# Performance work log

Hardware: AMD Instinct MI355X
Metric: run time of the kernel (lower is better)

Reference implementation:

```python
import jax, jax.numpy as jnp
import numpy as np

N_NOTES = 4096
SIZE = 64
N_EDGE_TYPE = 14  # len(GRAPH_KEYS) * 2
N_ITER = 5


def setup_inputs() -> dict:
    key = jax.random.key(0)
    ks = jax.random.split(key, 12)
    xav = np.sqrt(2.0 / (SIZE + SIZE))  # xavier_normal_ std for square [SIZE,SIZE]
    x = jax.random.normal(ks[0], (N_NOTES, SIZE), dtype=jnp.float32)
    # sparse binary adjacency per edge type (avg degree ~8) to keep gate
    # pre-activations in a sane range, as a real score graph would be
    edge_matrix = (jax.random.uniform(ks[1], (N_EDGE_TYPE, N_NOTES, N_NOTES)) < 0.002).astype(jnp.float32)
    wz = jax.random.normal(ks[2], (N_EDGE_TYPE, SIZE, SIZE), dtype=jnp.float32) * xav
    wr = jax.random.normal(ks[3], (N_EDGE_TYPE, SIZE, SIZE), dtype=jnp.float32) * xav
    wh = jax.random.normal(ks[4], (N_EDGE_TYPE, SIZE, SIZE), dtype=jnp.float32) * xav
    uz = jax.random.normal(ks[5], (SIZE, SIZE), dtype=jnp.float32) * xav
    ur = jax.random.normal(ks[6], (SIZE, SIZE), dtype=jnp.float32) * xav
    uh = jax.random.normal(ks[7], (SIZE, SIZE), dtype=jnp.float32) * xav
    bz = jnp.zeros((SIZE,), dtype=jnp.float32)
    br = jnp.zeros((SIZE,), dtype=jnp.float32)
    bh = jnp.zeros((SIZE,), dtype=jnp.float32)
    return {"x": x, "edge_matrix": edge_matrix, "wz": wz, "wr": wr, "wh": wh,
            "uz": uz, "ur": ur, "uh": uh, "bz": bz, "br": br, "bh": bh}


def reference(x, edge_matrix, wz, wr, wh, uz, ur, uh, bz, br, bh):
    # Faithful GatedGraph.forward: 5 iterations of edge-typed message passing
    # with GRU-style gates and the (unusual, but as-written) blend
    #   h <- (1 - z) * h + r * h_tilde
    h = x  # [N, D]
    for _ in range(N_ITER):
        # activation[e, n, d] = sum_m edge[e, m, n] * h[m, d]  (edge_matrix.transpose(1,2) @ h)
        act = jnp.einsum('emn,md->end', edge_matrix, h)  # [E, N, D]
        az = jnp.einsum('end,edf->nf', act, wz)  # bmm(act, wz).sum(0)
        ar = jnp.einsum('end,edf->nf', act, wr)
        ah = jnp.einsum('end,edf->nf', act, wh)
        z = jax.nn.sigmoid(az + h @ uz + bz)
        r = jax.nn.sigmoid(ar + h @ ur + br)
        h_tilde = jnp.tanh(ah + (r * h) @ uh + bh)
        h = (1.0 - z) * h + r * h_tilde
    return h
```

## Files before the change

### kernel.cpp

```cpp
#include <hip/hip_runtime.h>
#include <hip/hip_bf16.h>
#include <cstdint>

#define N_NOTES 4096
#define SIZE 64
#define NE 14
#define NITER 5
#define MAXDEG 64
#define KTOT 960
#define ASTR 968
#define HPAD 4113
#define PWN 184320
#define PUN 4096

typedef __attribute__((ext_vector_type(8))) short short8;
typedef __attribute__((ext_vector_type(4))) float float4v;

__device__ __forceinline__ ushort f2bf(float f){
  union{float f; uint32_t u;} x; x.f=f;
  uint32_t r = x.u + 0x7fffu + ((x.u>>16)&1u);
  return (ushort)(r>>16);
}
__device__ __forceinline__ float bf2f(ushort h){
  union{uint32_t u; float f;} x; x.u=((uint32_t)h)<<16; return x.f;
}
__device__ __forceinline__ void split_bf(float v, ushort& hi, ushort& lo){
  hi = f2bf(v);
  lo = f2bf(v - bf2f(hi));
}

__global__ __launch_bounds__(256) void k_zero(int* __restrict__ deg, uint32_t* __restrict__ adj32,
                                              float* __restrict__ h0pad, float* __restrict__ h1pad){
  int i = blockIdx.x*256 + threadIdx.x;
  if (i < NE*N_NOTES) deg[i] = 0;
  for (int j = i; j < NE*N_NOTES*MAXDEG/2; j += gridDim.x*256)
    adj32[j] = 0x10101010u;
  if (i < (HPAD-N_NOTES)*SIZE){ h0pad[i] = 0.f; h1pad[i] = 0.f; }
}

__global__ __launch_bounds__(256) void k_build(const float4v* __restrict__ edge4,
                                               int* __restrict__ deg,
                                               ushort* __restrict__ adj){
  int row = blockIdx.x;
  int e = row >> 12, m = row & 4095;
  const float4v* p = edge4 + (size_t)row * (N_NOTES/4);
  int t = threadIdx.x;
  #pragma unroll
  for (int i=0;i<4;i++){
    int idx4 = t + i*256;
    float4v v = p[idx4];
    int nbase = idx4*4;
    #pragma unroll
    for (int j=0;j<4;j++){
      if (v[j] != 0.0f){
        int n = nbase + j;
        int slot = atomicAdd(&deg[(e<<12)+n], 1);
        if (slot < MAXDEG) adj[(size_t)((e<<12)+n)*MAXDEG + slot] = (ushort)m;
      }
    }
  }
}

__global__ __launch_bounds__(256) void k_pack(const float* __restrict__ wz, const float* __restrict__ wr,
                                              const float* __restrict__ wh, const float* __restrict__ uz,
                                              const float* __restrict__ ur, const float* __restrict__ uh,
                                              ushort* __restrict__ PWH, ushort* __restrict__ PWL,
                                              ushort* __restrict__ PUH, ushort* __restrict__ PUL){
  int idx = blockIdx.x*256 + threadIdx.x;
  if (idx < PWN){
    int j = idx & 7, lane = (idx>>3)&63, t = idx>>9;
    int kk = t % 30, wg = t/30; int w = wg & 3, g = wg >> 2;
    int col = g*64 + w*16 + (lane&15);
    int k = kk*32 + ((lane>>4)<<3) + j;
    int e = k >> 6, d = k & 63, f = col & 63;
    float v;
    if (e < NE){
      const float* wp = (g==0)?wz:(g==1)?wr:wh;
      v = wp[(e*64 + d)*64 + f];
    } else {
      v = (g==0) ? uz[d*64+f] : (g==1) ? ur[d*64+f] : 0.0f;
    }
    ushort hi,lo; split_bf(v,hi,lo);
    PWH[idx]=hi; PWL[idx]=lo;
  } else if (idx < PWN + PUN){
    int i2 = idx - PWN;
    int j = i2 & 7, lane = (i2>>3)&63, t = i2>>9;
    int kk = t & 1, w = t >> 1;
    int col = w*16 + (lane&15);
    int k = kk*32 + ((lane>>4)<<3) + j;
    float v = uh[k*64 + col];
    ushort hi,lo; split_bf(v,hi,lo);
    PUH[i2]=hi; PUL[i2]=lo;
  }
}

__global__ __launch_bounds__(256) void k_fused(const int* __restrict__ deg, const ushort* __restrict__ adj,
                                               const ushort* __restrict__ PWH, const ushort* __restrict__ PWL,
                                               const ushort* __restrict__ PUH, const ushort* __restrict__ PUL,
                                               const float* __restrict__ bz, const float* __restrict__ br,
                                               const float* __restrict__ bh,
                                               const float* __restrict__ hin, float* __restrict__ hout,
                                               float* __restrict__ out, int last){
  __shared__ ushort aHs[16*ASTR];
  __shared__ ushort aLs[16*ASTR];

  const int tid  = threadIdx.x;
  const int w    = tid >> 6;
  const int lane = tid & 63;
  const int qi   = lane >> 4;
  const int ql   = lane & 15;
  const int r0   = blockIdx.x * 16;
  const float4v* hin4 = (const float4v*)hin;

  const int ri = w*4 + qi;
  const int n  = r0 + ri;

  int dgv[NE]; int mvv[NE];
  #pragma unroll
  for (int e=0;e<NE;e++){
    int base = (e<<12) + n;
    dgv[e] = deg[base];
    mvv[e] = adj[(size_t)base*MAXDEG + ql];
  }
  #pragma unroll
  for (int p=0; p<15; ++p){
    float4v a0={0.f,0.f,0.f,0.f}, a1={0.f,0.f,0.f,0.f};
    float4v a2={0.f,0.f,0.f,0.f}, a3={0.f,0.f,0.f,0.f};
    if (p < NE){
      #pragma unroll
      for (int k=0;k<16;k+=4){
        int m0 = __shfl(mvv[p], qi*16 + k);
        int m1 = __shfl(mvv[p], qi*16 + k+1);
        int m2 = __shfl(mvv[p], qi*16 + k+2);
        int m3 = __shfl(mvv[p], qi*16 + k+3);
        a0 += hin4[m0*16 + ql];
        a1 += hin4[m1*16 + ql];
        a2 += hin4[m2*16 + ql];
        a3 += hin4[m3*16 + ql];
      }
      int dg = dgv[p];
      if (dg > 16){
        size_t base = (size_t)((p<<12)+n)*MAXDEG;
        for (int k=16;k<dg;k++){
          int m = adj[base + k];
          a0 += hin4[m*16 + ql];
        }
      }
    } else {
      a0 = hin4[n*16 + ql];
    }
    float4v acc = (a0 + a1) + (a2 + a3);
    ushort h0,h1,h2,h3,l0,l1,l2,l3;
    split_bf(acc[0],h0,l0); split_bf(acc[1],h1,l1);
    split_bf(acc[2],h2,l2); split_bf(acc[3],h3,l3);
    int o = ri*ASTR + p*64 + ql*4;
    *(ushort4*)&aHs[o] = make_ushort4(h0,h1,h2,h3);
    *(ushort4*)&aLs[o] = make_ushort4(l0,l1,l2,l3);
  }
  __syncthreads();

  const int l15  = lane & 15;
  const int koff = (lane >> 4) * 8;
  const int colf = w*16 + l15;
  float4v acc[3];
  #pragma unroll
  for (int g=0;g<3;g++) acc[g] = (float4v){0.f,0.f,0.f,0.f};
  #pragma unroll 3
  for (int kk=0; kk<30; ++kk){
    short8 aH = *(const short8*)&aHs[l15*ASTR + kk*32 + koff];
    short8 aL = *(const short8*)&aLs[l15*ASTR + kk*32 + koff];
    #pragma unroll
    for (int g=0; g<3; ++g){
      int boff = (((g*4 + w)*30 + kk) << 9) + lane*8;
      short8 bH = *(const short8*)(PWH + boff);
      short8 bL = *(const short8*)(PWL + boff);
      acc[g] = __builtin_amdgcn_mfma_f32_16x16x32_bf16(aH,bH,acc[g],0,0,0);
      acc[g] = __builtin_amdgcn_mfma_f32_16x16x32_bf16(aH,bL,acc[g],0,0,0);
      acc[g] = __builtin_amdgcn_mfma_f32_16x16x32_bf16(aL,bH,acc[g],0,0,0);
    }
  }
  __syncthreads();

  ushort* rhH = aHs;
  ushort* rhL = aHs + 16*72;
  const int crow0 = (lane>>4)*4;
  const float brf = br[colf];
  float hrow[4], rreg[4];
  #pragma unroll
  for (int i=0;i<4;i++){
    float hv = hin[(size_t)(r0+crow0+i)*64 + colf];
    hrow[i] = hv;
    float r = 1.f/(1.f + expf(-(acc[1][i] + brf)));
    rreg[i] = r;
    ushort hi,lo; split_bf(r*hv,hi,lo);
    rhH[(crow0+i)*72 + colf] = hi;
    rhL[(crow0+i)*72 + colf] = lo;
  }
  __syncthreads();

  float4v acc2 = {0.f,0.f,0.f,0.f};
  #pragma unroll
  for (int kk=0; kk<2; ++kk){
    short8 aH = *(const short8*)&rhH[l15*72 + kk*32 + koff];
    short8 aL = *(const short8*)&rhL[l15*72 + kk*32 + koff];
    int boff = (((w<<1) + kk) << 9) + lane*8;
    short8 bH = *(const short8*)(PUH + boff);
    short8 bL = *(const short8*)(PUL + boff);
    acc2 = __builtin_amdgcn_mfma_f32_16x16x32_bf16(aH,bH,acc2,0,0,0);
    acc2 = __builtin_amdgcn_mfma_f32_16x16x32_bf16(aH,bL,acc2,0,0,0);
    acc2 = __builtin_amdgcn_mfma_f32_16x16x32_bf16(aL,bH,acc2,0,0,0);
  }

  const float bzf = bz[colf], bhf = bh[colf];
  #pragma unroll
  for (int i=0;i<4;i++){
    float z  = 1.f/(1.f + expf(-(acc[0][i] + bzf)));
    float ht = tanhf(acc[2][i] + acc2[i] + bhf);
    float hn = (1.f - z)*hrow[i] + rreg[i]*ht;
    size_t idx = (size_t)(r0+crow0+i)*64 + colf;
    hout[idx] = hn;
    if (last) out[idx] = hn;
  }
}

extern "C" void kernel_launch(void* const* d_in, const int* in_sizes, int n_in,
                              void* d_out, int out_size, void* d_ws, size_t ws_size,
                              hipStream_t stream) {
  const float* x    = (const float*)d_in[0];
  const float* edge = (const float*)d_in[1];
  const float* wz   = (const float*)d_in[2];
  const float* wr   = (const float*)d_in[3];
  const float* wh   = (const float*)d_in[4];
  const float* uz   = (const float*)d_in[5];
  const float* ur   = (const float*)d_in[6];
  const float* uh   = (const float*)d_in[7];
  const float* bz   = (const float*)d_in[8];
  const float* br   = (const float*)d_in[9];
  const float* bh   = (const float*)d_in[10];
  float* out = (float*)d_out;

  char* ws = (char*)d_ws;
  size_t off = 0;
  auto alloc = [&](size_t bytes)->void*{
    void* p = ws + off;
    off = (off + bytes + 255) & ~(size_t)255;
    return p;
  };
  const size_t EN = (size_t)NE * N_NOTES;
  const size_t ND = (size_t)N_NOTES * SIZE;
  int*    deg  = (int*)   alloc(EN * 4);
  ushort* adj  = (ushort*)alloc(EN * MAXDEG * 2);
  ushort* PWH  = (ushort*)alloc((size_t)PWN * 2);
  ushort* PWL  = (ushort*)alloc((size_t)PWN * 2);
  ushort* PUH  = (ushort*)alloc((size_t)PUN * 2);
  ushort* PUL  = (ushort*)alloc((size_t)PUN * 2);
  float*  h0   = (float*) alloc((size_t)HPAD * SIZE * 4);
  float*  h1   = (float*) alloc((size_t)HPAD * SIZE * 4);

  k_zero <<<2048, 256, 0, stream>>>(deg, (uint32_t*)adj,
                                    h0 + ND, h1 + ND);
  k_build<<<NE*N_NOTES, 256, 0, stream>>>((const float4v*)edge, deg, adj);
  k_pack <<<(PWN + PUN)/256, 256, 0, stream>>>(wz, wr, wh, uz, ur, uh, PWH, PWL, PUH, PUL);
  hipMemcpyAsync(h0, x, ND*4, hipMemcpyDeviceToDevice, stream);

  float* hcur = h0;
  float* hnxt = h1;
  for (int it = 0; it < NITER; ++it){
    k_fused<<<N_NOTES/16, 256, 0, stream>>>(deg, adj, PWH, PWL, PUH, PUL,
                                            bz, br, bh, hcur, hnxt,
                                            out, (it == NITER-1) ? 1 : 0);
    float* t = hcur; hcur = hnxt; hnxt = t;
  }
}
```

Measured before the change: 326.7 us.

## Split fused GRU step across 16 waves with K-split MFMA and LDS reduction

Grows the block from 4 to 16 waves per 16-row tile. The gather work of 240 (edge, row) pairs is spread across all waves, and the 30-step K loop of the gate GEMM is split four ways. Partial sums are then reduced through shared memory before the gate nonlinearities. This aims to raise parallelism and latency hiding per tile, at the cost of extra LDS traffic, two more barriers, and a tail where only 4 waves do the Uh MFMA and output.

After: 285.7 us. 12.6% less time.

```diff
diff --git a/kernel.cpp b/kernel.cpp
--- a/kernel.cpp
+++ b/kernel.cpp
@@ -12,6 +12,7 @@
 #define HPAD 4113
 #define PWN 184320
 #define PUN 4096
+#define PSTR 264
 
 typedef __attribute__((ext_vector_type(8))) short short8;
 typedef __attribute__((ext_vector_type(4))) float float4v;
@@ -69,8 +70,8 @@
   int idx = blockIdx.x*256 + threadIdx.x;
   if (idx < PWN){
     int j = idx & 7, lane = (idx>>3)&63, t = idx>>9;
-    int kk = t % 30, wg = t/30; int w = wg & 3, g = wg >> 2;
-    int col = g*64 + w*16 + (lane&15);
+    int kk = t % 30, wg = t/30; int cb = wg & 3, g = wg >> 2;
+    int col = g*64 + cb*16 + (lane&15);
     int k = kk*32 + ((lane>>4)<<3) + j;
     int e = k >> 6, d = k & 63, f = col & 63;
     float v;
@@ -85,8 +86,8 @@
   } else if (idx < PWN + PUN){
     int i2 = idx - PWN;
     int j = i2 & 7, lane = (i2>>3)&63, t = i2>>9;
-    int kk = t & 1, w = t >> 1;
-    int col = w*16 + (lane&15);
+    int kk = t & 1, cb = t >> 1;
+    int col = cb*16 + (lane&15);
     int k = kk*32 + ((lane>>4)<<3) + j;
     float v = uh[k*64 + col];
     ushort hi,lo; split_bf(v,hi,lo);
@@ -94,39 +95,53 @@
   }
 }
 
-__global__ __launch_bounds__(256) void k_fused(const int* __restrict__ deg, const ushort* __restrict__ adj,
-                                               const ushort* __restrict__ PWH, const ushort* __restrict__ PWL,
-                                               const ushort* __restrict__ PUH, const ushort* __restrict__ PUL,
-                                               const float* __restrict__ bz, const float* __restrict__ br,
-                                               const float* __restrict__ bh,
-                                               const float* __restrict__ hin, float* __restrict__ hout,
-                                               float* __restrict__ out, int last){
-  __shared__ ushort aHs[16*ASTR];
-  __shared__ ushort aLs[16*ASTR];
+__global__ __launch_bounds__(1024, 4)
+void k_fused(const int* __restrict__ deg, const ushort* __restrict__ adj,
+             const ushort* __restrict__ PWH, const ushort* __restrict__ PWL,
+             const ushort* __restrict__ PUH, const ushort* __restrict__ PUL,
+             const float* __restrict__ bz, const float* __restrict__ br,
+             const float* __restrict__ bh,
+             const float* __restrict__ hin, float* __restrict__ hout,
+             float* __restrict__ out, int last){
+  __shared__ ushort sh[31744];
+  ushort* aHs = sh;
+  ushort* aLs = sh + 16*ASTR;
+  float*  PSf = (float*)sh;
+  ushort* rhH = sh + 25344;
+  ushort* rhL = sh + 26496;
+  float*  zSf = (float*)(sh + 27648);
+  float*  rSf = (float*)(sh + 29696);
 
   const int tid  = threadIdx.x;
   const int w    = tid >> 6;
   const int lane = tid & 63;
   const int qi   = lane >> 4;
   const int ql   = lane & 15;
+  const int l15  = lane & 15;
+  const int koff = (lane >> 4) * 8;
   const int r0   = blockIdx.x * 16;
   const float4v* hin4 = (const float4v*)hin;
 
-  const int ri = w*4 + qi;
-  const int n  = r0 + ri;
-
-  int dgv[NE]; int mvv[NE];
-  #pragma unroll
-  for (int e=0;e<NE;e++){
-    int base = (e<<12) + n;
-    dgv[e] = deg[base];
-    mvv[e] = adj[(size_t)base*MAXDEG + ql];
-  }
-  #pragma unroll
-  for (int p=0; p<15; ++p){
+  const int Q = w*4 + qi;
+  int dgv[4], mvv[4];
+  #pragma unroll
+  for (int p=0;p<4;p++){
+    int u = p*64 + Q;
+    int e = u >> 4, n = r0 + (u & 15);
+    if (e < NE){
+      int base = (e<<12) + n;
+      dgv[p] = deg[base];
+      mvv[p] = adj[(size_t)base*MAXDEG + ql];
+    } else { dgv[p]=0; mvv[p]=0; }
+  }
+  #pragma unroll
+  for (int p=0;p<4;p++){
+    int u = p*64 + Q;
+    if (u >= 240) continue;
+    int e = u >> 4, ri = u & 15, n = r0 + ri;
     float4v a0={0.f,0.f,0.f,0.f}, a1={0.f,0.f,0.f,0.f};
     float4v a2={0.f,0.f,0.f,0.f}, a3={0.f,0.f,0.f,0.f};
-    if (p < NE){
+    if (e < NE){
       #pragma unroll
       for (int k=0;k<16;k+=4){
         int m0 = __shfl(mvv[p], qi*16 + k);
@@ -140,7 +155,7 @@
       }
       int dg = dgv[p];
       if (dg > 16){
-        size_t base = (size_t)((p<<12)+n)*MAXDEG;
+        size_t base = (size_t)((e<<12)+n)*MAXDEG;
         for (int k=16;k<dg;k++){
           int m = adj[base + k];
           a0 += hin4[m*16 + ql];
@@ -153,73 +168,98 @@
     ushort h0,h1,h2,h3,l0,l1,l2,l3;
     split_bf(acc[0],h0,l0); split_bf(acc[1],h1,l1);
     split_bf(acc[2],h2,l2); split_bf(acc[3],h3,l3);
-    int o = ri*ASTR + p*64 + ql*4;
+    int o = ri*ASTR + e*64 + ql*4;
     *(ushort4*)&aHs[o] = make_ushort4(h0,h1,h2,h3);
     *(ushort4*)&aLs[o] = make_ushort4(l0,l1,l2,l3);
   }
   __syncthreads();
 
-  const int l15  = lane & 15;
-  const int koff = (lane >> 4) * 8;
-  const int colf = w*16 + l15;
+  const int cb = w & 3, kq = w >> 2;
+  const int kk0 = kq*8;
   float4v acc[3];
   #pragma unroll
   for (int g=0;g<3;g++) acc[g] = (float4v){0.f,0.f,0.f,0.f};
-  #pragma unroll 3
-  for (int kk=0; kk<30; ++kk){
-    short8 aH = *(const short8*)&aHs[l15*ASTR + kk*32 + koff];
-    short8 aL = *(const short8*)&aLs[l15*ASTR + kk*32 + koff];
-    #pragma unroll
-    for (int g=0; g<3; ++g){
-      int boff = (((g*4 + w)*30 + kk) << 9) + lane*8;
-      short8 bH = *(const short8*)(PWH + boff);
-      short8 bL = *(const short8*)(PWL + boff);
-      acc[g] = __builtin_amdgcn_mfma_f32_16x16x32_bf16(aH,bH,acc[g],0,0,0);
-      acc[g] = __builtin_amdgcn_mfma_f32_16x16x32_bf16(aH,bL,acc[g],0,0,0);
-      acc[g] = __builtin_amdgcn_mfma_f32_16x16x32_bf16(aL,bH,acc[g],0,0,0);
+  #pragma unroll
+  for (int kx=0; kx<8; ++kx){
+    int kk = kk0 + kx;
+    if (kk < 30){
+      short8 aH = *(const short8*)&aHs[l15*ASTR + kk*32 + koff];
+      short8 aL = *(const short8*)&aLs[l15*ASTR + kk*32 + koff];
+      #pragma unroll
+      for (int g=0; g<3; ++g){
+        int boff = (((g*4 + cb)*30 + kk) << 9) + lane*8;
+        short8 bH = *(const short8*)(PWH + boff);
+        short8 bL = *(const short8*)(PWL + boff);
+        acc[g] = __builtin_amdgcn_mfma_f32_16x16x32_bf16(aH,bH,acc[g],0,0,0);
+        acc[g] = __builtin_amdgcn_mfma_f32_16x16x32_bf16(aH,bL,acc[g],0,0,0);
+        acc[g] = __builtin_amdgcn_mfma_f32_16x16x32_bf16(aL,bH,acc[g],0,0,0);
+      }
     }
   }
   __syncthreads();
 
-  ushort* rhH = aHs;
-  ushort* rhL = aHs + 16*72;
-  const int crow0 = (lane>>4)*4;
-  const float brf = br[colf];
-  float hrow[4], rreg[4];
-  #pragma unroll
-  for (int i=0;i<4;i++){
-    float hv = hin[(size_t)(r0+crow0+i)*64 + colf];
-    hrow[i] = hv;
-    float r = 1.f/(1.f + expf(-(acc[1][i] + brf)));
-    rreg[i] = r;
-    ushort hi,lo; split_bf(r*hv,hi,lo);
-    rhH[(crow0+i)*72 + colf] = hi;
-    rhL[(crow0+i)*72 + colf] = lo;
+  {
+    int crow0 = (lane>>4)*4;
+    #pragma unroll
+    for (int g=0;g<3;g++){
+      float* slot = PSf + (size_t)(kq*12 + g*4 + cb)*PSTR;
+      #pragma unroll
+      for (int i=0;i<4;i++)
+        slot[(crow0+i)*16 + l15] = acc[g][i];
+    }
   }
   __syncthreads();
 
-  float4v acc2 = {0.f,0.f,0.f,0.f};
-  #pragma unroll
-  for (int kk=0; kk<2; ++kk){
-    short8 aH = *(const short8*)&rhH[l15*72 + kk*32 + koff];
-    short8 aL = *(const short8*)&rhL[l15*72 + kk*32 + koff];
-    int boff = (((w<<1) + kk) << 9) + lane*8;
-    short8 bH = *(const short8*)(PUH + boff);
-    short8 bL = *(const short8*)(PUL + boff);
-    acc2 = __builtin_amdgcn_mfma_f32_16x16x32_bf16(aH,bH,acc2,0,0,0);
-    acc2 = __builtin_amdgcn_mfma_f32_16x16x32_bf16(aH,bL,acc2,0,0,0);
-    acc2 = __builtin_amdgcn_mfma_f32_16x16x32_bf16(aL,bH,acc2,0,0,0);
-  }
-
-  const float bzf = bz[colf], bhf = bh[colf];
-  #pragma unroll
-  for (int i=0;i<4;i++){
-    float z  = 1.f/(1.f + expf(-(acc[0][i] + bzf)));
-    float ht = tanhf(acc[2][i] + acc2[i] + bhf);
-    float hn = (1.f - z)*hrow[i] + rreg[i]*ht;
-    size_t idx = (size_t)(r0+crow0+i)*64 + colf;
-    hout[idx] = hn;
-    if (last) out[idx] = hn;
+  {
+    int r = tid >> 6, f = tid & 63;
+    int cb2 = f >> 4, c = f & 15;
+    float az=0.f, ar=0.f, ah=0.f;
+    #pragma unroll
+    for (int k=0;k<4;k++){
+      az += PSf[(size_t)(k*12 + 0 + cb2)*PSTR + r*16 + c];
+      ar += PSf[(size_t)(k*12 + 4 + cb2)*PSTR + r*16 + c];
+      ah += PSf[(size_t)(k*12 + 8 + cb2)*PSTR + r*16 + c];
+    }
+    float z = 1.f/(1.f + expf(-(az + bz[f])));
+    float rg = 1.f/(1.f + expf(-(ar + br[f])));
+    float hv = hin[(size_t)(r0+r)*64 + f];
+    zSf[tid] = z;
+    rSf[tid] = rg;
+    ushort hi,lo; split_bf(rg*hv,hi,lo);
+    rhH[r*72+f] = hi;
+    rhL[r*72+f] = lo;
+    PSf[(size_t)(8 + cb2)*PSTR + r*16 + c] = ah;
+  }
+  __syncthreads();
+
+  if (w < 4){
+    const int colf = w*16 + l15;
+    float4v acc2 = {0.f,0.f,0.f,0.f};
+    #pragma unroll
+    for (int kk=0; kk<2; ++kk){
+      short8 aH = *(const short8*)&rhH[l15*72 + kk*32 + koff];
+      short8 aL = *(const short8*)&rhL[l15*72 + kk*32 + koff];
+      int boff = (((w<<1) + kk) << 9) + lane*8;
+      short8 bH = *(const short8*)(PUH + boff);
+      short8 bL = *(const short8*)(PUL + boff);
+      acc2 = __builtin_amdgcn_mfma_f32_16x16x32_bf16(aH,bH,acc2,0,0,0);
+      acc2 = __builtin_amdgcn_mfma_f32_16x16x32_bf16(aH,bL,acc2,0,0,0);
+      acc2 = __builtin_amdgcn_mfma_f32_16x16x32_bf16(aL,bH,acc2,0,0,0);
+    }
+    const int crow0 = (lane>>4)*4;
+    const float bhf = bh[colf];
+    #pragma unroll
+    for (int i=0;i<4;i++){
+      int row = crow0 + i;
+      float ah = PSf[(size_t)(8 + w)*PSTR + row*16 + l15];
+      float z  = zSf[row*64 + colf];
+      float rg = rSf[row*64 + colf];
+      float ht = tanhf(ah + acc2[i] + bhf);
+      size_t idx = (size_t)(r0+row)*64 + colf;
+      float hn = (1.f - z)*hin[idx] + rg*ht;
+      hout[idx] = hn;
+      if (last) out[idx] = hn;
+    }
   }
 }
 
@@ -257,8 +297,7 @@
   float*  h0   = (float*) alloc((size_t)HPAD * SIZE * 4);
   float*  h1   = (float*) alloc((size_t)HPAD * SIZE * 4);
 
-  k_zero <<<2048, 256, 0, stream>>>(deg, (uint32_t*)adj,
-                                    h0 + ND, h1 + ND);
+  k_zero <<<2048, 256, 0, stream>>>(deg, (uint32_t*)adj, h0 + ND, h1 + ND);
   k_build<<<NE*N_NOTES, 256, 0, stream>>>((const float4v*)edge, deg, adj);
   k_pack <<<(PWN + PUN)/256, 256, 0, stream>>>(wz, wr, wh, uz, ur, uh, PWH, PWL, PUH, PUL);
   hipMemcpyAsync(h0, x, ND*4, hipMemcpyDeviceToDevice, stream);
@@ -266,9 +305,9 @@
   float* hcur = h0;
   float* hnxt = h1;
   for (int it = 0; it < NITER; ++it){
-    k_fused<<<N_NOTES/16, 256, 0, stream>>>(deg, adj, PWH, PWL, PUH, PUL,
-                                            bz, br, bh, hcur, hnxt,
-                                            out, (it == NITER-1) ? 1 : 0);
+    k_fused<<<N_NOTES/16, 1024, 0, stream>>>(deg, adj, PWH, PWL, PUH, PUL,
+                                             bz, br, bh, hcur, hnxt,
+                                             out, (it == NITER-1) ? 1 : 0);
     float* t = hcur; hcur = hnxt; hnxt = t;
   }
 }
```
